# Optimization experiments

Hardware: AMD Instinct MI355X
Metric: run time of the kernel (lower is better)

The kernel has to match this reference:

```python
import jax, jax.numpy as jnp
import numpy as np

N_HEADS = 8


def setup_inputs() -> dict:
    key = jax.random.key(0)
    ks = jax.random.split(key, 12)
    B, C, H, W = 16, 256, 64, 64
    std = 1.0 / np.sqrt(C)  # init_std(conv) ~ 1/sqrt(fan_in) for a 1x1 conv
    return {
        "x": jax.random.normal(ks[0], (B, C, H, W), jnp.float32),
        "mod_multiplier": jax.random.normal(ks[1], (B, C), jnp.float32),
        "mod_bias": jax.random.normal(ks[2], (B, C), jnp.float32),
        "qkv_w": jax.random.normal(ks[3], (3 * C, C), jnp.float32) * std,
        "qkv_b": jnp.zeros((3 * C,), jnp.float32),
        "pe_q_h": jax.random.normal(ks[4], (1, C, H, 1), jnp.float32) * 0.02,
        "pe_q_w": jax.random.normal(ks[5], (1, C, 1, W), jnp.float32) * 0.02,
        "pe_k_h": jax.random.normal(ks[6], (1, C, H, 1), jnp.float32) * 0.02,
        "pe_k_w": jax.random.normal(ks[7], (1, C, 1, W), jnp.float32) * 0.02,
        "pre_act_bias": jnp.zeros((1, C, 1, 1), jnp.float32),
        "pre_qkv_bias": jnp.zeros((1, C, 1, 1), jnp.float32),
    }


def reference(x, mod_multiplier, mod_bias, qkv_w, qkv_b, pe_q_h, pe_q_w, pe_k_h, pe_k_w, pre_act_bias, pre_qkv_bias):
    B, C, H, W = x.shape
    hs = C // N_HEADS  # head_size
    dot_scale = jnp.asarray(hs, x.dtype) ** 0.5

    x_preact = jax.nn.silu(x + pre_act_bias)
    # 1x1 conv == channel GEMM: [B,C,H,W] x [3C,C] -> [B,3C,H,W]
    qkv = jnp.einsum('bchw,oc->bohw', x_preact + pre_qkv_bias, qkv_w) + qkv_b[None, :, None, None]
    q, k, v = jnp.split(qkv, 3, axis=1)

    q = q + pe_q_h + pe_q_w
    k = k + pe_k_h + pe_k_w
    q = q * mod_multiplier[:, :, None, None] + mod_bias[:, :, None, None]

    # view as [B, n_heads, head_size, H*W]
    q = q.reshape(B, N_HEADS, hs, H * W)
    k = k.reshape(B, N_HEADS, hs, H * W)
    v = v.reshape(B, N_HEADS, hs, H * W)

    # channel-attention: logits [B, n_heads, hs, hs]
    logits = jnp.einsum('bhcn,bhdn->bhcd', q, k) / dot_scale
    weights = jax.nn.softmax(logits, axis=-1)
    out = jnp.einsum('bhcd,bhdn->bhcn', weights, v).reshape(B, C, H, W)

    return jnp.concatenate((x_preact, out), axis=1)
```

## Files before the change

kernel.cpp:

```cpp
#include <hip/hip_runtime.h>

typedef short bf16x8 __attribute__((ext_vector_type(8)));
typedef float f32x4 __attribute__((ext_vector_type(4)));

__device__ __forceinline__ float b2f(unsigned short u) {
  union { unsigned int i; float f; } v; v.i = ((unsigned int)u) << 16; return v.f;
}
__device__ __forceinline__ unsigned short f2b(float f) {
  unsigned int u = __float_as_uint(f);
  u += 0x7fffu + ((u >> 16) & 1u);
  return (unsigned short)(u >> 16);
}
__device__ __forceinline__ float silu_f(float s) { return s / (1.0f + __expf(-s)); }

__device__ __forceinline__ void split2(float f, unsigned short& h, unsigned short& l) {
  h = f2b(f);
  l = f2b(f - b2f(h));
}

__device__ __forceinline__ void gload16(const unsigned short* g, unsigned short* l) {
  __builtin_amdgcn_global_load_lds(
      (const __attribute__((address_space(1))) unsigned int*)g,
      (__attribute__((address_space(3))) unsigned int*)l, 16, 0, 0);
}

__device__ __forceinline__ void unpack8(const unsigned* p, bf16x8& hi, bf16x8& lo) {
  uint4 a = *(const uint4*)p;
  uint4 b = *(const uint4*)(p + 4);
  unsigned u[8] = {a.x, a.y, a.z, a.w, b.x, b.y, b.z, b.w};
  unsigned hw[4], lw[4];
  #pragma unroll
  for (int j = 0; j < 4; j++) {
    hw[j] = __builtin_amdgcn_perm(u[2 * j + 1], u[2 * j], 0x05040100u);
    lw[j] = __builtin_amdgcn_perm(u[2 * j + 1], u[2 * j], 0x07060302u);
  }
  hi = *(bf16x8*)hw;
  lo = *(bf16x8*)lw;
}

__global__ __launch_bounds__(256) void k_wsplit(
    const float* __restrict__ W, unsigned short* __restrict__ Wh,
    unsigned short* __restrict__ Wl) {
  int e = (blockIdx.x * 256 + threadIdx.x) * 8;
  float4 a = *(const float4*)(W + e);
  float4 b = *(const float4*)(W + e + 4);
  float v[8] = {a.x, a.y, a.z, a.w, b.x, b.y, b.z, b.w};
  unsigned short h[8], l[8];
  #pragma unroll
  for (int j = 0; j < 8; j++) split2(v[j], h[j], l[j]);
  uint4 ph, pl;
  ph.x = h[0] | ((unsigned)h[1] << 16); ph.y = h[2] | ((unsigned)h[3] << 16);
  ph.z = h[4] | ((unsigned)h[5] << 16); ph.w = h[6] | ((unsigned)h[7] << 16);
  pl.x = l[0] | ((unsigned)l[1] << 16); pl.y = l[2] | ((unsigned)l[3] << 16);
  pl.z = l[4] | ((unsigned)l[5] << 16); pl.w = l[6] | ((unsigned)l[7] << 16);
  *(uint4*)(Wh + e) = ph;
  *(uint4*)(Wl + e) = pl;
}

__global__ __launch_bounds__(256) void k_prep(
    const float* __restrict__ x, const float* __restrict__ pab,
    const float* __restrict__ pqb, float* __restrict__ out) {
  __shared__ unsigned short th[64 * 64], tl[64 * 64];
  int blk = blockIdx.x;
  int nb = blk & 63;
  int cb = (blk >> 6) & 3;
  int b = blk >> 8;
  int n0 = nb * 64, c0 = cb * 64;
  int t = threadIdx.x;
  int nn = (t & 15) * 4;
  #pragma unroll
  for (int p = 0; p < 2; p++) {
    int c = 2 * (p * 16 + (t >> 4));
    float pa0 = pab[c0 + c], pq0 = pqb[c0 + c];
    float pa1 = pab[c0 + c + 1], pq1 = pqb[c0 + c + 1];
    float4 x0 = *(const float4*)(x + ((long long)(b * 256 + c0 + c)) * 4096 + n0 + nn);
    float4 x1 = *(const float4*)(x + ((long long)(b * 256 + c0 + c + 1)) * 4096 + n0 + nn);
    float t0[4] = {silu_f(x0.x + pa0) + pq0, silu_f(x0.y + pa0) + pq0,
                   silu_f(x0.z + pa0) + pq0, silu_f(x0.w + pa0) + pq0};
    float t1[4] = {silu_f(x1.x + pa1) + pq1, silu_f(x1.y + pa1) + pq1,
                   silu_f(x1.z + pa1) + pq1, silu_f(x1.w + pa1) + pq1};
    #pragma unroll
    for (int j = 0; j < 4; j++) {
      int nr = nn + j;
      unsigned short h0, l0, h1, l1;
      split2(t0[j], h0, l0);
      split2(t1[j], h1, l1);
      int pcol = ((((c >> 3) ^ (nr & 7)) << 3) | (c & 7));
      *(unsigned int*)(th + nr * 64 + pcol) = (unsigned)h0 | ((unsigned)h1 << 16);
      *(unsigned int*)(tl + nr * 64 + pcol) = (unsigned)l0 | ((unsigned)l1 << 16);
    }
  }
  __syncthreads();
  unsigned short* Th = (unsigned short*)(out + ((long long)(b * 512 + 256)) * 4096);
  unsigned short* Tl = Th + 4096 * 256;
  #pragma unroll
  for (int q = 0; q < 2; q++) {
    int s = q * 256 + t;
    int n = s >> 3, sc = s & 7;
    int psc = sc ^ (n & 7);
    uint4 vh = *(const uint4*)(th + n * 64 + psc * 8);
    uint4 vl = *(const uint4*)(tl + n * 64 + psc * 8);
    *(uint4*)(Th + (long long)(n0 + n) * 256 + c0 + sc * 8) = vh;
    *(uint4*)(Tl + (long long)(n0 + n) * 256 + c0 + sc * 8) = vl;
  }
}

__global__ __launch_bounds__(256) void k_act(
    const float* __restrict__ x, const float* __restrict__ pab,
    float* __restrict__ out) {
  long long e = ((long long)blockIdx.x * 256 + threadIdx.x) * 4;
  int b = (int)(e >> 20);
  int c = ((int)(e >> 12)) & 255;
  int n = (int)(e & 4095);
  float4 xv = *(const float4*)(x + e);
  float pa = pab[c];
  float4 o = {silu_f(xv.x + pa), silu_f(xv.y + pa), silu_f(xv.z + pa), silu_f(xv.w + pa)};
  *(float4*)(out + ((long long)(b * 512 + c)) * 4096 + n) = o;
}

template <int USE_LO>
__global__ __launch_bounds__(512, 4) void k_qkv(
    const unsigned short* __restrict__ Wh, const unsigned short* __restrict__ Wl,
    const float* __restrict__ qkvb,
    const float* __restrict__ peqh, const float* __restrict__ peqw,
    const float* __restrict__ pekh, const float* __restrict__ pekw,
    const float* __restrict__ modm, const float* __restrict__ modb,
    float* __restrict__ out, float* __restrict__ kv,
    int o_base, int obt) {
  extern __shared__ unsigned short sm[];
  const int BUFS = USE_LO ? 16384 : 8192;

  int bx = blockIdx.x;
  int nb = bx & 31;
  int hb = bx >> 5;
  int ob = hb % obt;
  int b = hb / obt;
  int o0 = o_base + ob * 128, n0 = nb * 128;
  int t = threadIdx.x;
  int lane = t & 63, w = t >> 6;
  int wm = w >> 2, wn = w & 3;
  int l15 = lane & 15, l4 = lane >> 4;

  const unsigned short* Th =
      (const unsigned short*)(out + ((long long)(b * 512 + 256)) * 4096);
  const unsigned short* Tl = Th + 4096 * 256;

  const unsigned short* src;
  int dstoff, row0;
  if (USE_LO) {
    int p = w >> 1, hh = w & 1;
    src = (p == 0) ? Wh : (p == 1) ? Wl : (p == 2) ? Th : Tl;
    row0 = ((p < 2) ? o0 : n0) + hh * 64;
    dstoff = p * 4096 + hh * 2048;
  } else {
    int p = w >> 2, qq = w & 3;
    src = (p == 0) ? Wh : Th;
    row0 = ((p == 0) ? o0 : n0) + qq * 32;
    dstoff = p * 4096 + qq * 1024;
  }
  const int nI = USE_LO ? 4 : 2;
  int laneoff = (lane >> 2) * 256 + (((lane & 3) ^ ((lane >> 3) & 3)) << 3);
  const unsigned short* sbase = src + (long long)row0 * 256 + laneoff;

  f32x4 z = {0.f, 0.f, 0.f, 0.f};
  f32x4 acc[4][2];
  #pragma unroll
  for (int i = 0; i < 4; i++)
    #pragma unroll
    for (int j = 0; j < 2; j++) acc[i][j] = z;

  int sw = (l4 ^ ((l15 >> 1) & 3)) << 3;

  #pragma unroll
  for (int i = 0; i < nI; i++) gload16(sbase + i * 4096, sm + dstoff + i * 512);

  int cur = 0;
  for (int step = 0; step < 8; ++step) {
    if (step < 7) {
      const unsigned short* sp = sbase + (step + 1) * 32;
      unsigned short* dp = sm + (cur ^ 1) * BUFS + dstoff;
      #pragma unroll
      for (int i = 0; i < nI; i++) gload16(sp + i * 4096, dp + i * 512);
      if (USE_LO) asm volatile("s_waitcnt vmcnt(4)" ::: "memory");
      else        asm volatile("s_waitcnt vmcnt(2)" ::: "memory");
    } else {
      asm volatile("s_waitcnt vmcnt(0)" ::: "memory");
    }
    __builtin_amdgcn_s_barrier();
    __builtin_amdgcn_sched_barrier(0);
    unsigned short* Ah = sm + cur * BUFS;
    unsigned short* Al = Ah + 4096;
    unsigned short* Bh = Ah + (USE_LO ? 8192 : 4096);
    unsigned short* Bl = Ah + 12288;
    bf16x8 ah[4], al[4], bh[2], bl[2];
    #pragma unroll
    for (int i = 0; i < 4; i++) {
      int rowA = (wm * 64 + i * 16 + l15) * 32;
      ah[i] = *(const bf16x8*)(Ah + rowA + sw);
      if (USE_LO) al[i] = *(const bf16x8*)(Al + rowA + sw);
    }
    #pragma unroll
    for (int j = 0; j < 2; j++) {
      int rowB = (wn * 32 + j * 16 + l15) * 32;
      bh[j] = *(const bf16x8*)(Bh + rowB + sw);
      if (USE_LO) bl[j] = *(const bf16x8*)(Bl + rowB + sw);
    }
    #pragma unroll
    for (int i = 0; i < 4; i++)
      #pragma unroll
      for (int j = 0; j < 2; j++) {
        acc[i][j] = __builtin_amdgcn_mfma_f32_16x16x32_bf16(ah[i], bh[j], acc[i][j], 0, 0, 0);
        if (USE_LO) {
          acc[i][j] = __builtin_amdgcn_mfma_f32_16x16x32_bf16(ah[i], bl[j], acc[i][j], 0, 0, 0);
          acc[i][j] = __builtin_amdgcn_mfma_f32_16x16x32_bf16(al[i], bh[j], acc[i][j], 0, 0, 0);
        }
      }
    __builtin_amdgcn_sched_barrier(0);
    __builtin_amdgcn_s_barrier();
    cur ^= 1;
  }

  int part = o0 >> 8;
  #pragma unroll
  for (int i = 0; i < 4; i++) {
    #pragma unroll
    for (int r = 0; r < 4; r++) {
      int o = o0 + wm * 64 + i * 16 + l4 * 4 + r;
      int cch = o & 255;
      float bias = qkvb[o];
      float mm = 0.f, mb = 0.f;
      if (part == 0) { mm = modm[b * 256 + cch]; mb = modb[b * 256 + cch]; }
      #pragma unroll
      for (int j = 0; j < 2; j++) {
        int n = n0 + wn * 32 + j * 16 + l15;
        float v = acc[i][j][r] + bias;
        int hh = n >> 6, ww = n & 63;
        if (part == 0) {
          v += peqh[cch * 64 + hh] + peqw[cch * 64 + ww];
          v = v * mm + mb;
          unsigned short h, l; split2(v, h, l);
          ((unsigned*)out)[((long long)(b * 512 + cch)) * 4096 + n] =
              (unsigned)h | ((unsigned)l << 16);
        } else if (part == 1) {
          v += pekh[cch * 64 + hh] + pekw[cch * 64 + ww];
          unsigned short h, l; split2(v, h, l);
          ((unsigned*)kv)[((long long)(b * 256 + cch)) * 4096 + n] =
              (unsigned)h | ((unsigned)l << 16);
        } else {
          kv[((long long)(b * 256 + cch)) * 4096 + n] = v;
        }
      }
    }
  }
}

__global__ __launch_bounds__(256) void k_logits(
    const unsigned* __restrict__ qp, const unsigned* __restrict__ kp,
    float* __restrict__ logitsP) {
  int bx = blockIdx.x;
  int chunk = bx & 3, bh = bx >> 2;
  int b = bh >> 3, h = bh & 7;
  int t = threadIdx.x, lane = t & 63, w = t >> 6;
  int l15 = lane & 15, l4 = lane >> 4;
  const unsigned* qb = qp + ((long long)(b * 512 + h * 32)) * 4096;
  const unsigned* kb = kp + ((long long)(b * 256 + h * 32)) * 4096;
  f32x4 z = {0.f, 0.f, 0.f, 0.f};
  f32x4 acc[2][2] = {z, z, z, z};
  int nstep0 = chunk * 1024 + w * 256;
  for (int it = 0; it < 8; it++) {
    int n = nstep0 + it * 32 + l4 * 8;
    bf16x8 qh0, ql0, qh1, ql1, kh0, kl0, kh1, kl1;
    unpack8(qb + (long long)l15 * 4096 + n, qh0, ql0);
    unpack8(qb + (long long)(16 + l15) * 4096 + n, qh1, ql1);
    unpack8(kb + (long long)l15 * 4096 + n, kh0, kl0);
    unpack8(kb + (long long)(16 + l15) * 4096 + n, kh1, kl1);
    acc[0][0] = __builtin_amdgcn_mfma_f32_16x16x32_bf16(qh0, kh0, acc[0][0], 0, 0, 0);
    acc[0][0] = __builtin_amdgcn_mfma_f32_16x16x32_bf16(qh0, kl0, acc[0][0], 0, 0, 0);
    acc[0][0] = __builtin_amdgcn_mfma_f32_16x16x32_bf16(ql0, kh0, acc[0][0], 0, 0, 0);
    acc[0][1] = __builtin_amdgcn_mfma_f32_16x16x32_bf16(qh0, kh1, acc[0][1], 0, 0, 0);
    acc[0][1] = __builtin_amdgcn_mfma_f32_16x16x32_bf16(qh0, kl1, acc[0][1], 0, 0, 0);
    acc[0][1] = __builtin_amdgcn_mfma_f32_16x16x32_bf16(ql0, kh1, acc[0][1], 0, 0, 0);
    acc[1][0] = __builtin_amdgcn_mfma_f32_16x16x32_bf16(qh1, kh0, acc[1][0], 0, 0, 0);
    acc[1][0] = __builtin_amdgcn_mfma_f32_16x16x32_bf16(qh1, kl0, acc[1][0], 0, 0, 0);
    acc[1][0] = __builtin_amdgcn_mfma_f32_16x16x32_bf16(ql1, kh0, acc[1][0], 0, 0, 0);
    acc[1][1] = __builtin_amdgcn_mfma_f32_16x16x32_bf16(qh1, kh1, acc[1][1], 0, 0, 0);
    acc[1][1] = __builtin_amdgcn_mfma_f32_16x16x32_bf16(qh1, kl1, acc[1][1], 0, 0, 0);
    acc[1][1] = __builtin_amdgcn_mfma_f32_16x16x32_bf16(ql1, kh1, acc[1][1], 0, 0, 0);
  }
  __shared__ float red[4][1024];
  #pragma unroll
  for (int ch = 0; ch < 2; ch++)
    #pragma unroll
    for (int dh = 0; dh < 2; dh++)
      #pragma unroll
      for (int r = 0; r < 4; r++) {
        int crow = ch * 16 + l4 * 4 + r;
        int dcol = dh * 16 + l15;
        red[w][crow * 32 + dcol] = acc[ch][dh][r];
      }
  __syncthreads();
  const float scale = 0.1767766952966369f;
  #pragma unroll
  for (int i = 0; i < 4; i++) {
    int idx = i * 256 + t;
    float s = (red[0][idx] + red[1][idx] + red[2][idx] + red[3][idx]) * scale;
    logitsP[(long long)chunk * 131072 + bh * 1024 + idx] = s;
  }
}

__global__ __launch_bounds__(256) void k_pv(
    const float* __restrict__ kv,
    const float* __restrict__ logitsP,
    float* __restrict__ out) {
  int bx = blockIdx.x;
  int ntile = bx & 15, bh = bx >> 4;
  int b = bh >> 3, h = bh & 7;
  int t = threadIdx.x;
  __shared__ float raw[32][33];
  __shared__ float wsm[32][33];
  #pragma unroll
  for (int i = 0; i < 4; i++) {
    int idx = i * 256 + t;
    float s = logitsP[bh * 1024 + idx] + logitsP[131072 + bh * 1024 + idx]
            + logitsP[262144 + bh * 1024 + idx] + logitsP[393216 + bh * 1024 + idx];
    raw[idx >> 5][idx & 31] = s;
  }
  __syncthreads();
  if (t < 32) {
    float mx = -1e30f;
    for (int d = 0; d < 32; d++) mx = fmaxf(mx, raw[t][d]);
    float e[32]; float s = 0.f;
    for (int d = 0; d < 32; d++) { e[d] = __expf(raw[t][d] - mx); s += e[d]; }
    float inv = 1.0f / s;
    for (int d = 0; d < 32; d++) wsm[t][d] = e[d] * inv;
  }
  __syncthreads();
  int rg = t >> 6;
  int nl = (t & 63) * 4;
  int n0 = ntile * 256 + nl;
  const float* vb = kv + ((long long)(b * 256 + h * 32)) * 4096 + n0;
  float acc[8][4];
  #pragma unroll
  for (int r = 0; r < 8; r++)
    #pragma unroll
    for (int i = 0; i < 4; i++) acc[r][i] = 0.f;
  for (int d = 0; d < 32; d++) {
    float4 vv = *(const float4*)(vb + (long long)d * 4096);
    #pragma unroll
    for (int r = 0; r < 8; r++) {
      float wv = wsm[rg * 8 + r][d];
      acc[r][0] += wv * vv.x; acc[r][1] += wv * vv.y;
      acc[r][2] += wv * vv.z; acc[r][3] += wv * vv.w;
    }
  }
  #pragma unroll
  for (int r = 0; r < 8; r++) {
    long long oidx = ((long long)(b * 512 + 256 + h * 32 + rg * 8 + r)) * 4096 + n0;
    float4 ov = {acc[r][0], acc[r][1], acc[r][2], acc[r][3]};
    *(float4*)(out + oidx) = ov;
  }
}

extern "C" void kernel_launch(void* const* d_in, const int* in_sizes, int n_in,
                              void* d_out, int out_size, void* d_ws, size_t ws_size,
                              hipStream_t stream) {
  const float* x    = (const float*)d_in[0];
  const float* modm = (const float*)d_in[1];
  const float* modb = (const float*)d_in[2];
  const float* Wq   = (const float*)d_in[3];
  const float* qkvb = (const float*)d_in[4];
  const float* peqh = (const float*)d_in[5];
  const float* peqw = (const float*)d_in[6];
  const float* pekh = (const float*)d_in[7];
  const float* pekw = (const float*)d_in[8];
  const float* pab  = (const float*)d_in[9];
  const float* pqb  = (const float*)d_in[10];
  float* out = (float*)d_out;

  unsigned short* Wh = (unsigned short*)d_ws;
  unsigned short* Wl = Wh + 768 * 256;
  float* logitsP = (float*)((char*)d_ws + (1 << 20));
  float* kv = (float*)((char*)d_ws + 3 * (1 << 20));

  k_wsplit<<<96, 256, 0, stream>>>(Wq, Wh, Wl);
  k_prep<<<4096, 256, 0, stream>>>(x, pab, pqb, out);
  k_qkv<1><<<2048, 512, 65536, stream>>>(Wh, Wl, qkvb, peqh, peqw, pekh, pekw,
                                         modm, modb, out, kv, 0, 4);
  k_logits<<<512, 256, 0, stream>>>((const unsigned*)out, (const unsigned*)kv, logitsP);
  k_qkv<0><<<1024, 512, 32768, stream>>>(Wh, Wl, qkvb, peqh, peqw, pekh, pekw,
                                         modm, modb, out, kv, 512, 2);
  k_pv<<<2048, 256, 0, stream>>>(kv, logitsP, out);
  k_act<<<16384, 256, 0, stream>>>(x, pab, out);
}
```

Before: 378.5 us.

## Fuse Q/K projection with logits and fold activation output into prep

Adds a kernel that computes the Q and K projections for a 128-column tile and immediately forms the per-head 32x32 logits partials from shared memory. The partials are accumulated into a zeroed buffer with atomics, so Q and K are never written to or read back from global memory. The separate activation kernel is removed: the prep kernel now writes the SiLU output while it builds the transposed split-bf16 operand. The cost is many atomic adds from 32 tiles per head, plus a memset launch, and the atomics make the float summation order nondeterministic.

```diff
diff --git a/kernel.cpp b/kernel.cpp
--- a/kernel.cpp
+++ b/kernel.cpp
@@ -75,10 +75,16 @@
     float pa1 = pab[c0 + c + 1], pq1 = pqb[c0 + c + 1];
     float4 x0 = *(const float4*)(x + ((long long)(b * 256 + c0 + c)) * 4096 + n0 + nn);
     float4 x1 = *(const float4*)(x + ((long long)(b * 256 + c0 + c + 1)) * 4096 + n0 + nn);
-    float t0[4] = {silu_f(x0.x + pa0) + pq0, silu_f(x0.y + pa0) + pq0,
-                   silu_f(x0.z + pa0) + pq0, silu_f(x0.w + pa0) + pq0};
-    float t1[4] = {silu_f(x1.x + pa1) + pq1, silu_f(x1.y + pa1) + pq1,
-                   silu_f(x1.z + pa1) + pq1, silu_f(x1.w + pa1) + pq1};
+    float s0[4] = {silu_f(x0.x + pa0), silu_f(x0.y + pa0),
+                   silu_f(x0.z + pa0), silu_f(x0.w + pa0)};
+    float s1[4] = {silu_f(x1.x + pa1), silu_f(x1.y + pa1),
+                   silu_f(x1.z + pa1), silu_f(x1.w + pa1)};
+    float4 sv0 = {s0[0], s0[1], s0[2], s0[3]};
+    float4 sv1 = {s1[0], s1[1], s1[2], s1[3]};
+    *(float4*)(out + ((long long)(b * 512 + c0 + c)) * 4096 + n0 + nn) = sv0;
+    *(float4*)(out + ((long long)(b * 512 + c0 + c + 1)) * 4096 + n0 + nn) = sv1;
+    float t0[4] = {s0[0] + pq0, s0[1] + pq0, s0[2] + pq0, s0[3] + pq0};
+    float t1[4] = {s1[0] + pq1, s1[1] + pq1, s1[2] + pq1, s1[3] + pq1};
     #pragma unroll
     for (int j = 0; j < 4; j++) {
       int nr = nn + j;
@@ -105,17 +111,156 @@
   }
 }
 
-__global__ __launch_bounds__(256) void k_act(
-    const float* __restrict__ x, const float* __restrict__ pab,
-    float* __restrict__ out) {
-  long long e = ((long long)blockIdx.x * 256 + threadIdx.x) * 4;
-  int b = (int)(e >> 20);
-  int c = ((int)(e >> 12)) & 255;
-  int n = (int)(e & 4095);
-  float4 xv = *(const float4*)(x + e);
-  float pa = pab[c];
-  float4 o = {silu_f(xv.x + pa), silu_f(xv.y + pa), silu_f(xv.z + pa), silu_f(xv.w + pa)};
-  *(float4*)(out + ((long long)(b * 512 + c)) * 4096 + n) = o;
+__global__ __launch_bounds__(256) void k_qkl(
+    const unsigned short* __restrict__ Wh, const unsigned short* __restrict__ Wl,
+    const float* __restrict__ qkvb,
+    const float* __restrict__ peqh, const float* __restrict__ peqw,
+    const float* __restrict__ pekh, const float* __restrict__ pekw,
+    const float* __restrict__ modm, const float* __restrict__ modb,
+    const float* __restrict__ outT, float* __restrict__ logits) {
+  __shared__ __align__(16) unsigned short stg[12288];
+  __shared__ __align__(16) unsigned qk[64 * 128];
+  int bx = blockIdx.x;
+  int ntile = bx & 31, h = (bx >> 5) & 7, b = bx >> 8;
+  int n0 = ntile * 128;
+  int t = threadIdx.x, lane = t & 63, w = t >> 6;
+  int l15 = lane & 15, l4 = lane >> 4;
+
+  const unsigned short* Th =
+      (const unsigned short*)(outT + ((long long)(b * 512 + 256)) * 4096);
+  const unsigned short* Tl = Th + 4096 * 256;
+
+  const unsigned short* csrc[6];
+  unsigned short* cdst[6];
+  int lrow = lane >> 2;
+  int lslot = ((lane & 3) ^ ((lane >> 3) & 3)) * 8;
+  #pragma unroll
+  for (int i = 0; i < 6; i++) {
+    int c = w * 6 + i;
+    const unsigned short* plane;
+    int rowb, ldsoff;
+    if (c < 8) {
+      plane = (c & 4) ? Wl : Wh;
+      int sub = c & 3;
+      rowb = h * 32 + ((sub & 2) ? 256 : 0) + (sub & 1) * 16;
+      ldsoff = c * 512;
+    } else {
+      int ci = c - 8;
+      plane = (ci & 8) ? Tl : Th;
+      rowb = n0 + (ci & 7) * 16;
+      ldsoff = 4096 + ci * 512;
+    }
+    csrc[i] = plane + (long long)(rowb + lrow) * 256 + lslot;
+    cdst[i] = stg + ldsoff;
+  }
+
+  int sw = (l4 ^ ((l15 >> 1) & 3)) << 3;
+  f32x4 z = {0.f, 0.f, 0.f, 0.f};
+  f32x4 acc[4][2];
+  #pragma unroll
+  for (int i = 0; i < 4; i++)
+    #pragma unroll
+    for (int j = 0; j < 2; j++) acc[i][j] = z;
+
+  for (int step = 0; step < 8; ++step) {
+    int k0 = step * 32;
+    #pragma unroll
+    for (int i = 0; i < 6; i++) gload16(csrc[i] + k0, cdst[i]);
+    __syncthreads();
+    bf16x8 ah[4], al[4], bh[2], bl[2];
+    #pragma unroll
+    for (int i = 0; i < 4; i++) {
+      int ro = (i * 16 + l15) * 32 + sw;
+      ah[i] = *(const bf16x8*)(stg + ro);
+      al[i] = *(const bf16x8*)(stg + 2048 + ro);
+    }
+    #pragma unroll
+    for (int j = 0; j < 2; j++) {
+      int ro = (w * 32 + j * 16 + l15) * 32 + sw;
+      bh[j] = *(const bf16x8*)(stg + 4096 + ro);
+      bl[j] = *(const bf16x8*)(stg + 8192 + ro);
+    }
+    #pragma unroll
+    for (int i = 0; i < 4; i++)
+      #pragma unroll
+      for (int j = 0; j < 2; j++) {
+        acc[i][j] = __builtin_amdgcn_mfma_f32_16x16x32_bf16(ah[i], bh[j], acc[i][j], 0, 0, 0);
+        acc[i][j] = __builtin_amdgcn_mfma_f32_16x16x32_bf16(ah[i], bl[j], acc[i][j], 0, 0, 0);
+        acc[i][j] = __builtin_amdgcn_mfma_f32_16x16x32_bf16(al[i], bh[j], acc[i][j], 0, 0, 0);
+      }
+    __syncthreads();
+  }
+
+  int b256 = b * 256;
+  #pragma unroll
+  for (int i = 0; i < 4; i++) {
+    #pragma unroll
+    for (int r = 0; r < 4; r++) {
+      int row = i * 16 + l4 * 4 + r;
+      int cch = h * 32 + (row & 31);
+      float bias = qkvb[(row & 32) ? (256 + cch) : cch];
+      float mm = 0.f, mb = 0.f;
+      if (row < 32) { mm = modm[b256 + cch]; mb = modb[b256 + cch]; }
+      #pragma unroll
+      for (int j = 0; j < 2; j++) {
+        int nl = w * 32 + j * 16 + l15;
+        int n = n0 + nl;
+        int hh = n >> 6, ww = n & 63;
+        float v = acc[i][j][r] + bias;
+        if (row < 32) {
+          v += peqh[cch * 64 + hh] + peqw[cch * 64 + ww];
+          v = v * mm + mb;
+        } else {
+          v += pekh[cch * 64 + hh] + pekw[cch * 64 + ww];
+        }
+        unsigned short hi_, lo_;
+        split2(v, hi_, lo_);
+        int pch = (nl >> 3) ^ (row & 15);
+        qk[row * 128 + pch * 8 + (nl & 7)] = (unsigned)hi_ | ((unsigned)lo_ << 16);
+      }
+    }
+  }
+  __syncthreads();
+
+  f32x4 acc2[2][2] = {z, z, z, z};
+  int chn = w * 4 + l4;
+  bf16x8 qh[2], ql[2], kh[2], kl[2];
+  #pragma unroll
+  for (int i2 = 0; i2 < 2; i2++) {
+    int row = i2 * 16 + l15;
+    unpack8(qk + row * 128 + ((chn ^ l15) << 3), qh[i2], ql[i2]);
+    unpack8(qk + (row + 32) * 128 + ((chn ^ l15) << 3), kh[i2], kl[i2]);
+  }
+  acc2[0][0] = __builtin_amdgcn_mfma_f32_16x16x32_bf16(qh[0], kh[0], acc2[0][0], 0, 0, 0);
+  acc2[0][0] = __builtin_amdgcn_mfma_f32_16x16x32_bf16(qh[0], kl[0], acc2[0][0], 0, 0, 0);
+  acc2[0][0] = __builtin_amdgcn_mfma_f32_16x16x32_bf16(ql[0], kh[0], acc2[0][0], 0, 0, 0);
+  acc2[0][1] = __builtin_amdgcn_mfma_f32_16x16x32_bf16(qh[0], kh[1], acc2[0][1], 0, 0, 0);
+  acc2[0][1] = __builtin_amdgcn_mfma_f32_16x16x32_bf16(qh[0], kl[1], acc2[0][1], 0, 0, 0);
+  acc2[0][1] = __builtin_amdgcn_mfma_f32_16x16x32_bf16(ql[0], kh[1], acc2[0][1], 0, 0, 0);
+  acc2[1][0] = __builtin_amdgcn_mfma_f32_16x16x32_bf16(qh[1], kh[0], acc2[1][0], 0, 0, 0);
+  acc2[1][0] = __builtin_amdgcn_mfma_f32_16x16x32_bf16(qh[1], kl[0], acc2[1][0], 0, 0, 0);
+  acc2[1][0] = __builtin_amdgcn_mfma_f32_16x16x32_bf16(ql[1], kh[0], acc2[1][0], 0, 0, 0);
+  acc2[1][1] = __builtin_amdgcn_mfma_f32_16x16x32_bf16(qh[1], kh[1], acc2[1][1], 0, 0, 0);
+  acc2[1][1] = __builtin_amdgcn_mfma_f32_16x16x32_bf16(qh[1], kl[1], acc2[1][1], 0, 0, 0);
+  acc2[1][1] = __builtin_amdgcn_mfma_f32_16x16x32_bf16(ql[1], kh[1], acc2[1][1], 0, 0, 0);
+
+  float* red = (float*)stg;
+  #pragma unroll
+  for (int i2 = 0; i2 < 2; i2++)
+    #pragma unroll
+    for (int j2 = 0; j2 < 2; j2++)
+      #pragma unroll
+      for (int r = 0; r < 4; r++)
+        red[w * 1024 + (i2 * 16 + l4 * 4 + r) * 32 + j2 * 16 + l15] = acc2[i2][j2][r];
+  __syncthreads();
+  const float scale = 0.1767766952966369f;
+  int bhid = b * 8 + h;
+  #pragma unroll
+  for (int i = 0; i < 4; i++) {
+    int idx = i * 256 + t;
+    float s = (red[idx] + red[1024 + idx] + red[2048 + idx] + red[3072 + idx]) * scale;
+    atomicAdd(logits + (long long)bhid * 1024 + idx, s);
+  }
 }
 
 template <int USE_LO>
@@ -254,63 +399,9 @@
   }
 }
 
-__global__ __launch_bounds__(256) void k_logits(
-    const unsigned* __restrict__ qp, const unsigned* __restrict__ kp,
-    float* __restrict__ logitsP) {
-  int bx = blockIdx.x;
-  int chunk = bx & 3, bh = bx >> 2;
-  int b = bh >> 3, h = bh & 7;
-  int t = threadIdx.x, lane = t & 63, w = t >> 6;
-  int l15 = lane & 15, l4 = lane >> 4;
-  const unsigned* qb = qp + ((long long)(b * 512 + h * 32)) * 4096;
-  const unsigned* kb = kp + ((long long)(b * 256 + h * 32)) * 4096;
-  f32x4 z = {0.f, 0.f, 0.f, 0.f};
-  f32x4 acc[2][2] = {z, z, z, z};
-  int nstep0 = chunk * 1024 + w * 256;
-  for (int it = 0; it < 8; it++) {
-    int n = nstep0 + it * 32 + l4 * 8;
-    bf16x8 qh0, ql0, qh1, ql1, kh0, kl0, kh1, kl1;
-    unpack8(qb + (long long)l15 * 4096 + n, qh0, ql0);
-    unpack8(qb + (long long)(16 + l15) * 4096 + n, qh1, ql1);
-    unpack8(kb + (long long)l15 * 4096 + n, kh0, kl0);
-    unpack8(kb + (long long)(16 + l15) * 4096 + n, kh1, kl1);
-    acc[0][0] = __builtin_amdgcn_mfma_f32_16x16x32_bf16(qh0, kh0, acc[0][0], 0, 0, 0);
-    acc[0][0] = __builtin_amdgcn_mfma_f32_16x16x32_bf16(qh0, kl0, acc[0][0], 0, 0, 0);
-    acc[0][0] = __builtin_amdgcn_mfma_f32_16x16x32_bf16(ql0, kh0, acc[0][0], 0, 0, 0);
-    acc[0][1] = __builtin_amdgcn_mfma_f32_16x16x32_bf16(qh0, kh1, acc[0][1], 0, 0, 0);
-    acc[0][1] = __builtin_amdgcn_mfma_f32_16x16x32_bf16(qh0, kl1, acc[0][1], 0, 0, 0);
-    acc[0][1] = __builtin_amdgcn_mfma_f32_16x16x32_bf16(ql0, kh1, acc[0][1], 0, 0, 0);
-    acc[1][0] = __builtin_amdgcn_mfma_f32_16x16x32_bf16(qh1, kh0, acc[1][0], 0, 0, 0);
-    acc[1][0] = __builtin_amdgcn_mfma_f32_16x16x32_bf16(qh1, kl0, acc[1][0], 0, 0, 0);
-    acc[1][0] = __builtin_amdgcn_mfma_f32_16x16x32_bf16(ql1, kh0, acc[1][0], 0, 0, 0);
-    acc[1][1] = __builtin_amdgcn_mfma_f32_16x16x32_bf16(qh1, kh1, acc[1][1], 0, 0, 0);
-    acc[1][1] = __builtin_amdgcn_mfma_f32_16x16x32_bf16(qh1, kl1, acc[1][1], 0, 0, 0);
-    acc[1][1] = __builtin_amdgcn_mfma_f32_16x16x32_bf16(ql1, kh1, acc[1][1], 0, 0, 0);
-  }
-  __shared__ float red[4][1024];
-  #pragma unroll
-  for (int ch = 0; ch < 2; ch++)
-    #pragma unroll
-    for (int dh = 0; dh < 2; dh++)
-      #pragma unroll
-      for (int r = 0; r < 4; r++) {
-        int crow = ch * 16 + l4 * 4 + r;
-        int dcol = dh * 16 + l15;
-        red[w][crow * 32 + dcol] = acc[ch][dh][r];
-      }
-  __syncthreads();
-  const float scale = 0.1767766952966369f;
-  #pragma unroll
-  for (int i = 0; i < 4; i++) {
-    int idx = i * 256 + t;
-    float s = (red[0][idx] + red[1][idx] + red[2][idx] + red[3][idx]) * scale;
-    logitsP[(long long)chunk * 131072 + bh * 1024 + idx] = s;
-  }
-}
-
 __global__ __launch_bounds__(256) void k_pv(
     const float* __restrict__ kv,
-    const float* __restrict__ logitsP,
+    const float* __restrict__ logits,
     float* __restrict__ out) {
   int bx = blockIdx.x;
   int ntile = bx & 15, bh = bx >> 4;
@@ -321,9 +412,7 @@
   #pragma unroll
   for (int i = 0; i < 4; i++) {
     int idx = i * 256 + t;
-    float s = logitsP[bh * 1024 + idx] + logitsP[131072 + bh * 1024 + idx]
-            + logitsP[262144 + bh * 1024 + idx] + logitsP[393216 + bh * 1024 + idx];
-    raw[idx >> 5][idx & 31] = s;
+    raw[idx >> 5][idx & 31] = logits[(long long)bh * 1024 + idx];
   }
   __syncthreads();
   if (t < 32) {
@@ -379,16 +468,15 @@
 
   unsigned short* Wh = (unsigned short*)d_ws;
   unsigned short* Wl = Wh + 768 * 256;
-  float* logitsP = (float*)((char*)d_ws + (1 << 20));
+  float* logits = (float*)((char*)d_ws + (1 << 20));
   float* kv = (float*)((char*)d_ws + 3 * (1 << 20));
 
+  hipMemsetAsync(logits, 0, 16 * 8 * 32 * 32 * sizeof(float), stream);
   k_wsplit<<<96, 256, 0, stream>>>(Wq, Wh, Wl);
   k_prep<<<4096, 256, 0, stream>>>(x, pab, pqb, out);
-  k_qkv<1><<<2048, 512, 65536, stream>>>(Wh, Wl, qkvb, peqh, peqw, pekh, pekw,
-                                         modm, modb, out, kv, 0, 4);
-  k_logits<<<512, 256, 0, stream>>>((const unsigned*)out, (const unsigned*)kv, logitsP);
+  k_qkl<<<4096, 256, 0, stream>>>(Wh, Wl, qkvb, peqh, peqw, pekh, pekw,
+                                  modm, modb, out, logits);
   k_qkv<0><<<1024, 512, 32768, stream>>>(Wh, Wl, qkvb, peqh, peqw, pekh, pekw,
                                          modm, modb, out, kv, 512, 2);
-  k_pv<<<2048, 256, 0, stream>>>(kv, logitsP, out);
-  k_act<<<16384, 256, 0, stream>>>(x, pab, out);
-}
+  k_pv<<<2048, 256, 0, stream>>>(kv, logits, out);
+}
```

New measurement: 347.6 us. 8.2% less time.
